# Optimization experiments

Measured on AMD Instinct MI355X. Metric: run time of the kernel, lower is better.

## Reference

```python
import jax, jax.numpy as jnp
import numpy as np

B, T, O, N, M, H = 64, 128, 256, 65536, 64, 512
EPS = 1e-8


def setup_inputs() -> dict:
    key = jax.random.key(0)
    ks = jax.random.split(key, 8)
    x = jax.random.normal(ks[0], (B, T, O, 1), dtype=jnp.float32)
    # original: memory.uniform_(1e-05, 0.0001)
    memory0 = jax.random.uniform(ks[1], (N, M), dtype=jnp.float32, minval=1e-5, maxval=1e-4)
    eye = jnp.eye(B, N, dtype=jnp.float32)  # torch.eye(batch_size, N)
    h0 = jnp.zeros((B, H), dtype=jnp.float32)
    Wxh = jax.random.normal(ks[2], (O, H), dtype=jnp.float32) * 0.05
    Wrh = jax.random.normal(ks[3], (M, H), dtype=jnp.float32) * 0.1
    bh = jnp.zeros((H,), dtype=jnp.float32)
    Wo = jax.random.normal(ks[4], (H, O), dtype=jnp.float32) * 0.05
    bo = jnp.zeros((O,), dtype=jnp.float32)
    rW = jax.random.normal(ks[5], (H, M + 6), dtype=jnp.float32) * 0.05
    rb = jnp.zeros((M + 6,), dtype=jnp.float32)
    wW = jax.random.normal(ks[6], (H, 3 * M + 6), dtype=jnp.float32) * 0.05
    wb = jnp.zeros((3 * M + 6,), dtype=jnp.float32)
    return dict(x=x, memory0=memory0, wr=eye, ww=eye, h0=h0, Wxh=Wxh, Wrh=Wrh,
                bh=bh, Wo=Wo, bo=bo, rW=rW, rb=rb, wW=wW, wb=wb)


def _address(head_out, w_prev, mem):
    """Graves-2014 NTM addressing. head_out: (B, M+6) raw head projection."""
    k = jnp.tanh(head_out[:, :M])                          # key       (B, M)
    beta = jax.nn.softplus(head_out[:, M:M + 1])           # strength  (B, 1)
    g = jax.nn.sigmoid(head_out[:, M + 1:M + 2])           # gate      (B, 1)
    s = jax.nn.softmax(head_out[:, M + 2:M + 5], axis=-1)  # shift     (B, 3)
    gamma = 1.0 + jax.nn.softplus(head_out[:, M + 5:M + 6])  # sharpen (B, 1)
    kn = k / (jnp.linalg.norm(k, axis=-1, keepdims=True) + EPS)
    mn = mem / (jnp.linalg.norm(mem, axis=-1, keepdims=True) + EPS)
    wc = jax.nn.softmax(beta * (kn @ mn.T), axis=-1)       # content   (B, N)
    wg = g * wc + (1.0 - g) * w_prev                       # interpolate
    # circular shift conv over N with taps {-1, 0, +1}
    wt = (s[:, 0:1] * jnp.roll(wg, 1, axis=1)
          + s[:, 1:2] * wg
          + s[:, 2:3] * jnp.roll(wg, -1, axis=1))
    wp = (wt + EPS) ** gamma                               # sharpen
    return wp / jnp.sum(wp, axis=1, keepdims=True)


def reference(x, memory0, wr, ww, h0, Wxh, Wrh, bh, Wo, bo, rW, rb, wW, wb):
    xt = jnp.transpose(x, (1, 0, 2, 3)).reshape(T, B, O)  # time-major, flattened
    inv_b = 1.0 / B

    def step(carry, x_t):
        mem, h = carry
        # write head: address, then erase/add (memory shared across batch -> mean)
        wh = h @ wW + wb                                   # (B, 3M+6)
        w_w = _address(wh[:, :M + 6], ww, mem)             # (B, N)
        e = jax.nn.sigmoid(wh[:, M + 6:2 * M + 6])         # (B, M)
        a = jnp.tanh(wh[:, 2 * M + 6:3 * M + 6])           # (B, M)
        erase = jnp.einsum('bn,bm->nm', w_w, e) * inv_b    # (N, M)
        add = jnp.einsum('bn,bm->nm', w_w, a) * inv_b
        m_t = mem * (1.0 - erase) + add
        # read head
        rh = h @ rW + rb                                   # (B, M+6)
        w_r = _address(rh, wr, m_t)                        # (B, N)
        r_t = w_r @ m_t                                    # (B, M)
        # feedforward controller step + output
        h_new = jax.nn.relu(x_t @ Wxh + r_t @ Wrh + bh)    # (B, H)
        out = jax.nn.sigmoid(h_new @ Wo + bo)              # (B, O)
        return (m_t, h_new), out

    (_, _), outs = jax.lax.scan(step, (memory0, h0), xt)   # outs: (T, B, O)
    return jnp.transpose(outs, (1, 0, 2))                  # (B, T, O)
```

## Files before the change

kernel.cpp:

```cpp
#include <hip/hip_runtime.h>

#define NROWS 65536
#define BB 64
#define TT 128
#define OO 256
#define MM 64
#define HH 512
#define EPSF 1e-8f

__device__ __forceinline__ float wredsum(float v) {
#pragma unroll
  for (int o = 1; o < 64; o <<= 1) v += __shfl_xor(v, o, 64);
  return v;
}
__device__ __forceinline__ float sigm(float x) { return 1.f / (1.f + __expf(-x)); }
__device__ __forceinline__ float softplus_(float x) { return x > 20.f ? x : log1pf(__expf(x)); }

__global__ void __launch_bounds__(256) k_xpre(const float* __restrict__ x, const float* __restrict__ Wxh,
                                              const float* __restrict__ bh, float* __restrict__ Xpre) {
  __shared__ float xl[4][256];
  int tid = threadIdx.x;
#pragma unroll
  for (int i = 0; i < 4; ++i) {
    int pair = blockIdx.x * 4 + i;
    int t = pair >> 6, b = pair & 63;
    xl[i][tid] = x[((size_t)b * TT + t) * OO + tid];
  }
  __syncthreads();
  for (int u = 0; u < 2; ++u) {
    int hh = tid + u * 256;
    float a[4];
    float bv = bh[hh];
#pragma unroll
    for (int i = 0; i < 4; ++i) a[i] = bv;
    for (int o = 0; o < 256; ++o) {
      float wv = Wxh[(size_t)o * HH + hh];
#pragma unroll
      for (int i = 0; i < 4; ++i) a[i] += xl[i][o] * wv;
    }
#pragma unroll
    for (int i = 0; i < 4; ++i) {
      int pair = blockIdx.x * 4 + i;
      Xpre[(size_t)pair * HH + hh] = a[i];
    }
  }
}

__global__ void __launch_bounds__(256) k_w1(const float* __restrict__ msrc, const float* __restrict__ knwT,
                                            const float* __restrict__ prmw, float* __restrict__ E,
                                            float* __restrict__ Swst, float* __restrict__ S2rst) {
  int tid = threadIdx.x, blk = blockIdx.x;
  int base = blk * 64;
  __shared__ float rows[4096];
  __shared__ float sred[256];
  if (blk == 0) {
    for (int i = tid; i < 32 * 64; i += 256) S2rst[i] = 0.f;
  }
  {
    const float4* s4 = (const float4*)(msrc + (size_t)base * 64);
    float4* d4 = (float4*)rows;
#pragma unroll
    for (int i = 0; i < 4; ++i) d4[tid + i * 256] = s4[tid + i * 256];
  }
  int l = tid & 63, w = tid >> 6;
  float kr[64];
#pragma unroll
  for (int j = 0; j < 64; ++j) kr[j] = knwT[j * 64 + l];
  float beta = prmw[l * 8 + 0];
  __syncthreads();
  float sacc = 0.f;
  for (int r = w * 16; r < w * 16 + 16; ++r) {
    const float4* row4 = (const float4*)(rows + r * 64);
    float dot = 0.f, nsq = 0.f;
#pragma unroll
    for (int j = 0; j < 16; ++j) {
      float4 rv = row4[j];
      dot += kr[j * 4] * rv.x + kr[j * 4 + 1] * rv.y + kr[j * 4 + 2] * rv.z + kr[j * 4 + 3] * rv.w;
      nsq += rv.x * rv.x + rv.y * rv.y + rv.z * rv.z + rv.w * rv.w;
    }
    float ev = __expf(beta * dot / (sqrtf(nsq) + EPSF) - beta);
    E[(size_t)(base + r) * 64 + l] = ev;
    sacc += ev;
  }
  sred[tid] = sacc;
  __syncthreads();
  if (tid < 64)
    atomicAdd(&Swst[(blk & 31) * 64 + tid], sred[tid] + sred[tid + 64] + sred[tid + 128] + sred[tid + 192]);
}

__global__ void __launch_bounds__(256) k_w2(const float* __restrict__ E, const float* __restrict__ prmw,
                                            const float* __restrict__ Swst, float* __restrict__ wpg,
                                            float* __restrict__ S2wst) {
  int tid = threadIdx.x, blk = blockIdx.x, base = blk * 64;
  __shared__ float EL[66 * 64];
  __shared__ float Sw[64];
  __shared__ float sred[256];
  if (tid < 64) {
    float s = 0.f;
    for (int st = 0; st < 32; ++st) s += Swst[st * 64 + tid];
    Sw[tid] = s;
  }
  for (int i = tid; i < 66 * 64; i += 256) {
    int rr = i >> 6, b2 = i & 63;
    EL[i] = E[(size_t)((base - 1 + rr) & (NROWS - 1)) * 64 + b2];
  }
  __syncthreads();
  int b = tid & 63, w = tid >> 6;
  float g = prmw[b * 8 + 1], gam = prmw[b * 8 + 2];
  float s0 = prmw[b * 8 + 3], s1 = prmw[b * 8 + 4], s2 = prmw[b * 8 + 5];
  float gi = g / Sw[b], gm1 = 1.f - g;
  float s2acc = 0.f;
  for (int i = 0; i < 16; ++i) {
    int ln = w + i * 4;
    int n = base + ln;
    int nm = (n - 1) & (NROWS - 1), np = (n + 1) & (NROWS - 1);
    float wgm = gi * EL[ln * 64 + b] + (nm == b ? gm1 : 0.f);
    float wgc = gi * EL[(ln + 1) * 64 + b] + (n == b ? gm1 : 0.f);
    float wgp = gi * EL[(ln + 2) * 64 + b] + (np == b ? gm1 : 0.f);
    float wt = s0 * wgm + s1 * wgc + s2 * wgp;
    float wp = __powf(wt + EPSF, gam);
    wpg[(size_t)n * 64 + b] = wp;
    s2acc += wp;
  }
  sred[tid] = s2acc;
  __syncthreads();
  if (tid < 64)
    atomicAdd(&S2wst[(blk & 31) * 64 + tid], sred[tid] + sred[tid + 64] + sred[tid + 128] + sred[tid + 192]);
}

__global__ void __launch_bounds__(256) k_w3(const float* __restrict__ msrc, float* __restrict__ mdst,
                                            const float* __restrict__ wpg, const float* __restrict__ ea2,
                                            const float* __restrict__ knrT, const float* __restrict__ prmr,
                                            const float* __restrict__ S2wst, float* __restrict__ E,
                                            float* __restrict__ Srst) {
  int tid = threadIdx.x, blk = blockIdx.x, base = blk * 64;
  __shared__ float2 ealds[4096];
  __shared__ float wlT[4 * 64 * 20];
  __shared__ float rowsN[4096];
  __shared__ float fb[64];
  __shared__ float sred[256];
  {
    const float4* s4 = (const float4*)ea2;
    float4* d4 = (float4*)ealds;
#pragma unroll
    for (int i = 0; i < 8; ++i) d4[tid + i * 256] = s4[tid + i * 256];
  }
  if (tid < 64) {
    float s = 0.f;
    for (int st = 0; st < 32; ++st) s += S2wst[st * 64 + tid];
    fb[tid] = 1.f / (64.f * s);
  }
  __syncthreads();
  int l = tid & 63, w = tid >> 6;
#pragma unroll
  for (int k = 0; k < 16; ++k) {
    float wv = wpg[(size_t)(base + w * 16 + k) * 64 + l] * fb[l];
    wlT[(w * 64 + l) * 20 + k] = wv;
  }
  __syncthreads();
  float er[16], ad[16];
#pragma unroll
  for (int k = 0; k < 16; ++k) { er[k] = 0.f; ad[k] = 0.f; }
  for (int b2 = 0; b2 < 64; ++b2) {
    float2 eav = ealds[b2 * 64 + l];
    const float4* wrow = (const float4*)(wlT + (w * 64 + b2) * 20);
    float4 q0 = wrow[0], q1 = wrow[1], q2 = wrow[2], q3 = wrow[3];
    float qa[16];
    qa[0] = q0.x; qa[1] = q0.y; qa[2] = q0.z; qa[3] = q0.w;
    qa[4] = q1.x; qa[5] = q1.y; qa[6] = q1.z; qa[7] = q1.w;
    qa[8] = q2.x; qa[9] = q2.y; qa[10] = q2.z; qa[11] = q2.w;
    qa[12] = q3.x; qa[13] = q3.y; qa[14] = q3.z; qa[15] = q3.w;
#pragma unroll
    for (int k = 0; k < 16; ++k) { er[k] += qa[k] * eav.x; ad[k] += qa[k] * eav.y; }
  }
#pragma unroll
  for (int k = 0; k < 16; ++k) {
    int r = w * 16 + k;
    size_t n = (size_t)(base + r);
    float mv = msrc[n * 64 + l];
    float nv = mv * (1.f - er[k]) + ad[k];
    mdst[n * 64 + l] = nv;
    rowsN[r * 64 + l] = nv;
  }
  __syncthreads();
  float kr[64];
#pragma unroll
  for (int j = 0; j < 64; ++j) kr[j] = knrT[j * 64 + l];
  float beta_r = prmr[l * 8 + 0];
  float sacc = 0.f;
  for (int r = w * 16; r < w * 16 + 16; ++r) {
    const float4* row4 = (const float4*)(rowsN + r * 64);
    float dot = 0.f, nsq = 0.f;
#pragma unroll
    for (int j = 0; j < 16; ++j) {
      float4 rv = row4[j];
      dot += kr[j * 4] * rv.x + kr[j * 4 + 1] * rv.y + kr[j * 4 + 2] * rv.z + kr[j * 4 + 3] * rv.w;
      nsq += rv.x * rv.x + rv.y * rv.y + rv.z * rv.z + rv.w * rv.w;
    }
    float ev = __expf(beta_r * dot / (sqrtf(nsq) + EPSF) - beta_r);
    E[(size_t)(base + r) * 64 + l] = ev;
    sacc += ev;
  }
  sred[tid] = sacc;
  __syncthreads();
  if (tid < 64)
    atomicAdd(&Srst[(blk & 31) * 64 + tid], sred[tid] + sred[tid + 64] + sred[tid + 128] + sred[tid + 192]);
}

__global__ void __launch_bounds__(256) k_r2(const float* __restrict__ E, const float* __restrict__ mdst,
                                            const float* __restrict__ prmr, const float* __restrict__ Srst,
                                            float* __restrict__ part, float* __restrict__ S2rst) {
  int tid = threadIdx.x, blk = blockIdx.x, base = blk * 64;
  __shared__ float mt[4096];
  __shared__ float EL[66 * 64];
  __shared__ float Sr[64];
  __shared__ float sred[256];
  __shared__ float racc[64 * 65];
  if (tid < 64) {
    float s = 0.f;
    for (int st = 0; st < 32; ++st) s += Srst[st * 64 + tid];
    Sr[tid] = s;
  }
  {
    const float4* s4 = (const float4*)(mdst + (size_t)base * 64);
    float4* d4 = (float4*)mt;
#pragma unroll
    for (int i = 0; i < 4; ++i) d4[tid + i * 256] = s4[tid + i * 256];
  }
  for (int i = tid; i < 66 * 64; i += 256) {
    int rr = i >> 6, b2 = i & 63;
    EL[i] = E[(size_t)((base - 1 + rr) & (NROWS - 1)) * 64 + b2];
  }
  __syncthreads();
  int b = tid & 63, w = tid >> 6;
  float g = prmr[b * 8 + 1], gam = prmr[b * 8 + 2];
  float s0 = prmr[b * 8 + 3], s1 = prmr[b * 8 + 4], s2 = prmr[b * 8 + 5];
  float gi = g / Sr[b], gm1 = 1.f - g;
  float acc[64];
#pragma unroll
  for (int m = 0; m < 64; ++m) acc[m] = 0.f;
  float s2acc = 0.f;
  for (int i = 0; i < 16; ++i) {
    int r = w * 16 + i;
    int n = base + r;
    int nm = (n - 1) & (NROWS - 1), np = (n + 1) & (NROWS - 1);
    float wgm = gi * EL[r * 64 + b] + (nm == b ? gm1 : 0.f);
    float wgc = gi * EL[(r + 1) * 64 + b] + (n == b ? gm1 : 0.f);
    float wgp = gi * EL[(r + 2) * 64 + b] + (np == b ? gm1 : 0.f);
    float wt = s0 * wgm + s1 * wgc + s2 * wgp;
    float wp = __powf(wt + EPSF, gam);
    s2acc += wp;
    const float4* row4 = (const float4*)(mt + r * 64);
#pragma unroll
    for (int m4 = 0; m4 < 16; ++m4) {
      float4 mv = row4[m4];
      acc[m4 * 4 + 0] += wp * mv.x;
      acc[m4 * 4 + 1] += wp * mv.y;
      acc[m4 * 4 + 2] += wp * mv.z;
      acc[m4 * 4 + 3] += wp * mv.w;
    }
  }
  sred[tid] = s2acc;
  __syncthreads();
  if (tid < 64)
    atomicAdd(&S2rst[(blk & 31) * 64 + tid], sred[tid] + sred[tid + 64] + sred[tid + 128] + sred[tid + 192]);
  if (w == 0) {
#pragma unroll
    for (int m = 0; m < 64; ++m) racc[b * 65 + m] = acc[m];
  }
  __syncthreads();
  for (int ww2 = 1; ww2 < 4; ++ww2) {
    if (w == ww2) {
#pragma unroll
      for (int m = 0; m < 64; ++m) racc[b * 65 + m] += acc[m];
    }
    __syncthreads();
  }
  for (int i = tid; i < 4096; i += 256) part[(size_t)blk * 4096 + i] = racc[(i >> 6) * 65 + (i & 63)];
}

__global__ void __launch_bounds__(512) k_cp(int t, const float* __restrict__ h0,
                                            const float* __restrict__ Xpre, float* __restrict__ Hbuf,
                                            const float* __restrict__ part, const float* __restrict__ S2rst,
                                            const float* __restrict__ Wrh, const float* __restrict__ wW,
                                            const float* __restrict__ wb, const float* __restrict__ rW,
                                            const float* __restrict__ rb, float* __restrict__ knwT,
                                            float* __restrict__ knrT, float* __restrict__ ea2,
                                            float* __restrict__ prmw, float* __restrict__ prmr,
                                            float* __restrict__ zst) {
  int b = blockIdx.x, tid = threadIdx.x;
  __shared__ float hl[512];
  __shared__ float proj[268];
  __shared__ float red[512];
  __shared__ float rt[64];
  __shared__ float s2r_sh;
  if (t >= 0) {
    float v = 0.f;
    if (tid < 32) v = S2rst[tid * 64 + b];
    if (tid < 64) red[tid] = v;
    __syncthreads();
    if (tid == 0) {
      float s = 0.f;
      for (int i = 0; i < 32; ++i) s += red[i];
      s2r_sh = s;
    }
    __syncthreads();
    {
      int m = tid & 63, q = tid >> 6;
      float acc = 0.f;
      for (int p = q; p < 1024; p += 8) acc += part[((size_t)p * 64 + b) * 64 + m];
      red[tid] = acc;
    }
    __syncthreads();
    if (tid < 64) {
      float r = 0.f;
#pragma unroll
      for (int q8 = 0; q8 < 8; ++q8) r += red[tid + q8 * 64];
      rt[tid] = r / s2r_sh;
    }
    __syncthreads();
    {
      int hh = tid;
      float a = Xpre[((size_t)t * 64 + b) * HH + hh];
      for (int m2 = 0; m2 < 64; ++m2) a += rt[m2] * Wrh[(size_t)m2 * HH + hh];
      a = fmaxf(a, 0.f);
      Hbuf[((size_t)t * 64 + b) * HH + hh] = a;
      hl[hh] = a;
    }
  } else {
    hl[tid] = h0[(size_t)b * HH + tid];
  }
  __syncthreads();
  if (b == 0) {
    for (int i = tid; i < 3 * 2048; i += 512) zst[i] = 0.f;
  }
  if (tid < 268) {
    int idx = tid;
    float a;
    if (idx < 198) {
      a = wb[idx];
      for (int hh = 0; hh < 512; ++hh) a += hl[hh] * wW[(size_t)hh * 198 + idx];
    } else {
      int jj = idx - 198;
      a = rb[jj];
      for (int hh = 0; hh < 512; ++hh) a += hl[hh] * rW[(size_t)hh * 70 + jj];
    }
    proj[idx] = a;
  }
  __syncthreads();
  int l = tid & 63, wv = tid >> 6;
  if (wv == 0) {
    float kv = tanhf(proj[l]);
    float s = wredsum(kv * kv);
    knwT[l * 64 + b] = kv / (sqrtf(s) + EPSF);
  } else if (wv == 1) {
    float kv = tanhf(proj[198 + l]);
    float s = wredsum(kv * kv);
    knrT[l * 64 + b] = kv / (sqrtf(s) + EPSF);
  } else if (wv == 2) {
    float ev = sigm(proj[70 + l]);
    float av = tanhf(proj[134 + l]);
    ((float2*)ea2)[b * 64 + l] = make_float2(ev, av);
  } else if (wv == 3) {
    if (l == 0) {
      float beta = softplus_(proj[64]);
      float g = sigm(proj[65]);
      float v0 = proj[66], v1 = proj[67], v2 = proj[68];
      float mx = fmaxf(v0, fmaxf(v1, v2));
      float e0 = __expf(v0 - mx), e1 = __expf(v1 - mx), e2 = __expf(v2 - mx);
      float is = 1.f / (e0 + e1 + e2);
      float gam = 1.f + softplus_(proj[69]);
      prmw[b * 8 + 0] = beta; prmw[b * 8 + 1] = g; prmw[b * 8 + 2] = gam;
      prmw[b * 8 + 3] = e0 * is; prmw[b * 8 + 4] = e1 * is; prmw[b * 8 + 5] = e2 * is;
    } else if (l == 1) {
      const int of = 198;
      float beta = softplus_(proj[of + 64]);
      float g = sigm(proj[of + 65]);
      float v0 = proj[of + 66], v1 = proj[of + 67], v2 = proj[of + 68];
      float mx = fmaxf(v0, fmaxf(v1, v2));
      float e0 = __expf(v0 - mx), e1 = __expf(v1 - mx), e2 = __expf(v2 - mx);
      float is = 1.f / (e0 + e1 + e2);
      float gam = 1.f + softplus_(proj[of + 69]);
      prmr[b * 8 + 0] = beta; prmr[b * 8 + 1] = g; prmr[b * 8 + 2] = gam;
      prmr[b * 8 + 3] = e0 * is; prmr[b * 8 + 4] = e1 * is; prmr[b * 8 + 5] = e2 * is;
    }
  }
}

__global__ void __launch_bounds__(256) k_out(const float* __restrict__ Hbuf, const float* __restrict__ Wo,
                                             const float* __restrict__ bo, float* __restrict__ out) {
  __shared__ float hl[4][512];
  int tid = threadIdx.x;
#pragma unroll
  for (int i = 0; i < 8; ++i) {
    int idx = tid + i * 256;
    hl[idx >> 9][idx & 511] = Hbuf[(size_t)blockIdx.x * 2048 + idx];
  }
  __syncthreads();
  float a[4];
  float bv = bo[tid];
#pragma unroll
  for (int i = 0; i < 4; ++i) a[i] = bv;
  for (int hh = 0; hh < 512; ++hh) {
    float wv = Wo[(size_t)hh * OO + tid];
#pragma unroll
    for (int i = 0; i < 4; ++i) a[i] += hl[i][hh] * wv;
  }
#pragma unroll
  for (int i = 0; i < 4; ++i) {
    int pair = blockIdx.x * 4 + i;
    int t = pair >> 6, b = pair & 63;
    out[((size_t)b * TT + t) * OO + tid] = 1.f / (1.f + __expf(-a[i]));
  }
}

extern "C" void kernel_launch(void* const* d_in, const int* in_sizes, int n_in,
                              void* d_out, int out_size, void* d_ws, size_t ws_size,
                              hipStream_t stream) {
  (void)in_sizes; (void)n_in; (void)out_size; (void)ws_size;
  const float* x    = (const float*)d_in[0];
  const float* mem0 = (const float*)d_in[1];
  const float* h0   = (const float*)d_in[4];
  const float* Wxh  = (const float*)d_in[5];
  const float* Wrh  = (const float*)d_in[6];
  const float* bh   = (const float*)d_in[7];
  const float* Wo   = (const float*)d_in[8];
  const float* bo   = (const float*)d_in[9];
  const float* rW   = (const float*)d_in[10];
  const float* rb   = (const float*)d_in[11];
  const float* wW   = (const float*)d_in[12];
  const float* wb   = (const float*)d_in[13];
  float* ws = (float*)d_ws;
  const size_t NM = (size_t)NROWS * MM;
  float* memA = ws;
  float* memB = memA + NM;
  float* E    = memB + NM;
  float* wpg  = E + NM;
  float* Xpre = wpg + NM;
  float* Hbuf = Xpre + NM;
  float* part = Hbuf + NM;
  float* small = part + NM;
  float* knwT = small;
  float* knrT = knwT + 4096;
  float* ea2  = knrT + 4096;
  float* prmw = ea2 + 8192;
  float* prmr = prmw + 512;
  float* Swst  = prmr + 512;
  float* S2wst = Swst + 2048;
  float* Srst  = S2wst + 2048;
  float* S2rst = Srst + 2048;

  hipMemcpyAsync(memA, mem0, NM * sizeof(float), hipMemcpyDeviceToDevice, stream);
  k_xpre<<<2048, 256, 0, stream>>>(x, Wxh, bh, Xpre);
  k_cp<<<64, 512, 0, stream>>>(-1, h0, Xpre, Hbuf, part, S2rst, Wrh, wW, wb, rW, rb,
                               knwT, knrT, ea2, prmw, prmr, Swst);
  for (int t = 0; t < TT; ++t) {
    float* msrc = (t & 1) ? memB : memA;
    float* mdst = (t & 1) ? memA : memB;
    k_w1<<<1024, 256, 0, stream>>>(msrc, knwT, prmw, E, Swst, S2rst);
    k_w2<<<1024, 256, 0, stream>>>(E, prmw, Swst, wpg, S2wst);
    k_w3<<<1024, 256, 0, stream>>>(msrc, mdst, wpg, ea2, knrT, prmr, S2wst, E, Srst);
    k_r2<<<1024, 256, 0, stream>>>(E, mdst, prmr, Srst, part, S2rst);
    k_cp<<<64, 512, 0, stream>>>(t, h0, Xpre, Hbuf, part, S2rst, Wrh, wW, wb, rW, rb,
                                 knwT, knrT, ea2, prmw, prmr, Swst);
  }
  k_out<<<2048, 256, 0, stream>>>(Hbuf, Wo, bo, (float*)d_out);
}
```

Measured before the change: 25.10 ms.

## Recompute content weights in-block instead of storing E and wpg buffers

Drops the global wpg buffer and the E write in k_w3. k_w3 now recomputes the write-head content exponentials (with a one-row halo) and the sharpened weights from memory rows in shared memory. k_r2 likewise recomputes the read content exponentials from mdst rather than reading E. This trades extra dot-product and exp work, plus halo rows, for fewer full N×B global reads and writes per timestep, and reads ea2 straight from global memory instead of staging it in LDS.

```diff
diff --git a/kernel.cpp b/kernel.cpp
--- a/kernel.cpp
+++ b/kernel.cpp
@@ -89,8 +89,7 @@
 }
 
 __global__ void __launch_bounds__(256) k_w2(const float* __restrict__ E, const float* __restrict__ prmw,
-                                            const float* __restrict__ Swst, float* __restrict__ wpg,
-                                            float* __restrict__ S2wst) {
+                                            const float* __restrict__ Swst, float* __restrict__ S2wst) {
   int tid = threadIdx.x, blk = blockIdx.x, base = blk * 64;
   __shared__ float EL[66 * 64];
   __shared__ float Sw[64];
@@ -118,9 +117,7 @@
     float wgc = gi * EL[(ln + 1) * 64 + b] + (n == b ? gm1 : 0.f);
     float wgp = gi * EL[(ln + 2) * 64 + b] + (np == b ? gm1 : 0.f);
     float wt = s0 * wgm + s1 * wgc + s2 * wgp;
-    float wp = __powf(wt + EPSF, gam);
-    wpg[(size_t)n * 64 + b] = wp;
-    s2acc += wp;
+    s2acc += __powf(wt + EPSF, gam);
   }
   sred[tid] = s2acc;
   __syncthreads();
@@ -129,67 +126,31 @@
 }
 
 __global__ void __launch_bounds__(256) k_w3(const float* __restrict__ msrc, float* __restrict__ mdst,
-                                            const float* __restrict__ wpg, const float* __restrict__ ea2,
-                                            const float* __restrict__ knrT, const float* __restrict__ prmr,
-                                            const float* __restrict__ S2wst, float* __restrict__ E,
-                                            float* __restrict__ Srst) {
+                                            const float* __restrict__ ea2, const float* __restrict__ knwT,
+                                            const float* __restrict__ knrT, const float* __restrict__ prmw,
+                                            const float* __restrict__ prmr, const float* __restrict__ Swst,
+                                            const float* __restrict__ S2wst, float* __restrict__ Srst) {
   int tid = threadIdx.x, blk = blockIdx.x, base = blk * 64;
-  __shared__ float2 ealds[4096];
-  __shared__ float wlT[4 * 64 * 20];
-  __shared__ float rowsN[4096];
-  __shared__ float fb[64];
+  __shared__ float rows[66 * 64];
+  __shared__ float EL[66 * 64];
   __shared__ float sred[256];
-  {
-    const float4* s4 = (const float4*)ea2;
-    float4* d4 = (float4*)ealds;
-#pragma unroll
-    for (int i = 0; i < 8; ++i) d4[tid + i * 256] = s4[tid + i * 256];
-  }
-  if (tid < 64) {
-    float s = 0.f;
-    for (int st = 0; st < 32; ++st) s += S2wst[st * 64 + tid];
-    fb[tid] = 1.f / (64.f * s);
-  }
-  __syncthreads();
   int l = tid & 63, w = tid >> 6;
-#pragma unroll
-  for (int k = 0; k < 16; ++k) {
-    float wv = wpg[(size_t)(base + w * 16 + k) * 64 + l] * fb[l];
-    wlT[(w * 64 + l) * 20 + k] = wv;
-  }
-  __syncthreads();
-  float er[16], ad[16];
-#pragma unroll
-  for (int k = 0; k < 16; ++k) { er[k] = 0.f; ad[k] = 0.f; }
-  for (int b2 = 0; b2 < 64; ++b2) {
-    float2 eav = ealds[b2 * 64 + l];
-    const float4* wrow = (const float4*)(wlT + (w * 64 + b2) * 20);
-    float4 q0 = wrow[0], q1 = wrow[1], q2 = wrow[2], q3 = wrow[3];
-    float qa[16];
-    qa[0] = q0.x; qa[1] = q0.y; qa[2] = q0.z; qa[3] = q0.w;
-    qa[4] = q1.x; qa[5] = q1.y; qa[6] = q1.z; qa[7] = q1.w;
-    qa[8] = q2.x; qa[9] = q2.y; qa[10] = q2.z; qa[11] = q2.w;
-    qa[12] = q3.x; qa[13] = q3.y; qa[14] = q3.z; qa[15] = q3.w;
-#pragma unroll
-    for (int k = 0; k < 16; ++k) { er[k] += qa[k] * eav.x; ad[k] += qa[k] * eav.y; }
-  }
-#pragma unroll
-  for (int k = 0; k < 16; ++k) {
-    int r = w * 16 + k;
-    size_t n = (size_t)(base + r);
-    float mv = msrc[n * 64 + l];
-    float nv = mv * (1.f - er[k]) + ad[k];
-    mdst[n * 64 + l] = nv;
-    rowsN[r * 64 + l] = nv;
-  }
-  __syncthreads();
+  for (int i = tid; i < 66 * 64; i += 256) {
+    int rr = i >> 6, b2 = i & 63;
+    rows[i] = msrc[(size_t)((base - 1 + rr) & (NROWS - 1)) * 64 + b2];
+  }
   float kr[64];
 #pragma unroll
-  for (int j = 0; j < 64; ++j) kr[j] = knrT[j * 64 + l];
-  float beta_r = prmr[l * 8 + 0];
-  float sacc = 0.f;
-  for (int r = w * 16; r < w * 16 + 16; ++r) {
-    const float4* row4 = (const float4*)(rowsN + r * 64);
+  for (int j = 0; j < 64; ++j) kr[j] = knwT[j * 64 + l];
+  float beta = prmw[l * 8 + 0];
+  float Swl = 0.f, S2wl = 0.f;
+  for (int st = 0; st < 32; ++st) { Swl += Swst[st * 64 + l]; S2wl += S2wst[st * 64 + l]; }
+  __syncthreads();
+  for (int k = 0; k < 17; ++k) {
+    int r;
+    if (k < 16) r = w * 16 + k;
+    else { if (w >= 2) break; r = 64 + w; }
+    const float4* row4 = (const float4*)(rows + r * 64);
     float dot = 0.f, nsq = 0.f;
 #pragma unroll
     for (int j = 0; j < 16; ++j) {
@@ -197,9 +158,65 @@
       dot += kr[j * 4] * rv.x + kr[j * 4 + 1] * rv.y + kr[j * 4 + 2] * rv.z + kr[j * 4 + 3] * rv.w;
       nsq += rv.x * rv.x + rv.y * rv.y + rv.z * rv.z + rv.w * rv.w;
     }
-    float ev = __expf(beta_r * dot / (sqrtf(nsq) + EPSF) - beta_r);
-    E[(size_t)(base + r) * 64 + l] = ev;
-    sacc += ev;
+    EL[r * 64 + l] = __expf(beta * dot / (sqrtf(nsq) + EPSF) - beta);
+  }
+  __syncthreads();
+  float g = prmw[l * 8 + 1], gam = prmw[l * 8 + 2];
+  float s0 = prmw[l * 8 + 3], s1 = prmw[l * 8 + 4], s2 = prmw[l * 8 + 5];
+  float gi = g / Swl, gm1 = 1.f - g;
+  float fbl = 1.f / (64.f * S2wl);
+  float wpreg[16];
+#pragma unroll
+  for (int k = 0; k < 16; ++k) {
+    int r = w * 16 + k;
+    int n = base + r;
+    int nm = (n - 1) & (NROWS - 1), np = (n + 1) & (NROWS - 1);
+    float wgm = gi * EL[r * 64 + l] + (nm == l ? gm1 : 0.f);
+    float wgc = gi * EL[(r + 1) * 64 + l] + (n == l ? gm1 : 0.f);
+    float wgp = gi * EL[(r + 2) * 64 + l] + (np == l ? gm1 : 0.f);
+    float wt = s0 * wgm + s1 * wgc + s2 * wgp;
+    wpreg[k] = __powf(wt + EPSF, gam) * fbl;
+  }
+  __syncthreads();
+  float* wpn = EL;
+#pragma unroll
+  for (int k = 0; k < 16; ++k) wpn[(w * 16 + k) * 64 + l] = wpreg[k];
+  __syncthreads();
+  float er[16], ad[16];
+#pragma unroll
+  for (int k = 0; k < 16; ++k) { er[k] = 0.f; ad[k] = 0.f; }
+  for (int b2 = 0; b2 < 64; ++b2) {
+    float2 eav = ((const float2*)ea2)[b2 * 64 + l];
+#pragma unroll
+    for (int k = 0; k < 16; ++k) {
+      float wpb = wpn[(w * 16 + k) * 64 + b2];
+      er[k] += wpb * eav.x;
+      ad[k] += wpb * eav.y;
+    }
+  }
+#pragma unroll
+  for (int k = 0; k < 16; ++k) {
+    int r = w * 16 + k;
+    float mv = rows[(r + 1) * 64 + l];
+    float nv = mv * (1.f - er[k]) + ad[k];
+    mdst[(size_t)(base + r) * 64 + l] = nv;
+    rows[(r + 1) * 64 + l] = nv;
+  }
+  __syncthreads();
+#pragma unroll
+  for (int j = 0; j < 64; ++j) kr[j] = knrT[j * 64 + l];
+  float beta_r = prmr[l * 8 + 0];
+  float sacc = 0.f;
+  for (int k = 0; k < 16; ++k) {
+    const float4* row4 = (const float4*)(rows + (w * 16 + k + 1) * 64);
+    float dot = 0.f, nsq = 0.f;
+#pragma unroll
+    for (int j = 0; j < 16; ++j) {
+      float4 rv = row4[j];
+      dot += kr[j * 4] * rv.x + kr[j * 4 + 1] * rv.y + kr[j * 4 + 2] * rv.z + kr[j * 4 + 3] * rv.w;
+      nsq += rv.x * rv.x + rv.y * rv.y + rv.z * rv.z + rv.w * rv.w;
+    }
+    sacc += __expf(beta_r * dot / (sqrtf(nsq) + EPSF) - beta_r);
   }
   sred[tid] = sacc;
   __syncthreads();
@@ -207,35 +224,47 @@
     atomicAdd(&Srst[(blk & 31) * 64 + tid], sred[tid] + sred[tid + 64] + sred[tid + 128] + sred[tid + 192]);
 }
 
-__global__ void __launch_bounds__(256) k_r2(const float* __restrict__ E, const float* __restrict__ mdst,
+__global__ void __launch_bounds__(256) k_r2(const float* __restrict__ mdst, const float* __restrict__ knrT,
                                             const float* __restrict__ prmr, const float* __restrict__ Srst,
                                             float* __restrict__ part, float* __restrict__ S2rst) {
   int tid = threadIdx.x, blk = blockIdx.x, base = blk * 64;
-  __shared__ float mt[4096];
+  __shared__ float mt[66 * 64];
   __shared__ float EL[66 * 64];
   __shared__ float Sr[64];
   __shared__ float sred[256];
-  __shared__ float racc[64 * 65];
+  int l = tid & 63, w = tid >> 6;
+  for (int i = tid; i < 66 * 64; i += 256) {
+    int rr = i >> 6, b2 = i & 63;
+    mt[i] = mdst[(size_t)((base - 1 + rr) & (NROWS - 1)) * 64 + b2];
+  }
   if (tid < 64) {
     float s = 0.f;
     for (int st = 0; st < 32; ++st) s += Srst[st * 64 + tid];
     Sr[tid] = s;
   }
-  {
-    const float4* s4 = (const float4*)(mdst + (size_t)base * 64);
-    float4* d4 = (float4*)mt;
-#pragma unroll
-    for (int i = 0; i < 4; ++i) d4[tid + i * 256] = s4[tid + i * 256];
-  }
-  for (int i = tid; i < 66 * 64; i += 256) {
-    int rr = i >> 6, b2 = i & 63;
-    EL[i] = E[(size_t)((base - 1 + rr) & (NROWS - 1)) * 64 + b2];
-  }
-  __syncthreads();
-  int b = tid & 63, w = tid >> 6;
-  float g = prmr[b * 8 + 1], gam = prmr[b * 8 + 2];
-  float s0 = prmr[b * 8 + 3], s1 = prmr[b * 8 + 4], s2 = prmr[b * 8 + 5];
-  float gi = g / Sr[b], gm1 = 1.f - g;
+  float kr[64];
+#pragma unroll
+  for (int j = 0; j < 64; ++j) kr[j] = knrT[j * 64 + l];
+  float beta_r = prmr[l * 8 + 0];
+  __syncthreads();
+  for (int k = 0; k < 17; ++k) {
+    int r;
+    if (k < 16) r = w * 16 + k;
+    else { if (w >= 2) break; r = 64 + w; }
+    const float4* row4 = (const float4*)(mt + r * 64);
+    float dot = 0.f, nsq = 0.f;
+#pragma unroll
+    for (int j = 0; j < 16; ++j) {
+      float4 rv = row4[j];
+      dot += kr[j * 4] * rv.x + kr[j * 4 + 1] * rv.y + kr[j * 4 + 2] * rv.z + kr[j * 4 + 3] * rv.w;
+      nsq += rv.x * rv.x + rv.y * rv.y + rv.z * rv.z + rv.w * rv.w;
+    }
+    EL[r * 64 + l] = __expf(beta_r * dot / (sqrtf(nsq) + EPSF) - beta_r);
+  }
+  __syncthreads();
+  float g = prmr[l * 8 + 1], gam = prmr[l * 8 + 2];
+  float s0 = prmr[l * 8 + 3], s1 = prmr[l * 8 + 4], s2 = prmr[l * 8 + 5];
+  float gi = g / Sr[l], gm1 = 1.f - g;
   float acc[64];
 #pragma unroll
   for (int m = 0; m < 64; ++m) acc[m] = 0.f;
@@ -244,13 +273,13 @@
     int r = w * 16 + i;
     int n = base + r;
     int nm = (n - 1) & (NROWS - 1), np = (n + 1) & (NROWS - 1);
-    float wgm = gi * EL[r * 64 + b] + (nm == b ? gm1 : 0.f);
-    float wgc = gi * EL[(r + 1) * 64 + b] + (n == b ? gm1 : 0.f);
-    float wgp = gi * EL[(r + 2) * 64 + b] + (np == b ? gm1 : 0.f);
+    float wgm = gi * EL[r * 64 + l] + (nm == l ? gm1 : 0.f);
+    float wgc = gi * EL[(r + 1) * 64 + l] + (n == l ? gm1 : 0.f);
+    float wgp = gi * EL[(r + 2) * 64 + l] + (np == l ? gm1 : 0.f);
     float wt = s0 * wgm + s1 * wgc + s2 * wgp;
     float wp = __powf(wt + EPSF, gam);
     s2acc += wp;
-    const float4* row4 = (const float4*)(mt + r * 64);
+    const float4* row4 = (const float4*)(mt + (r + 1) * 64);
 #pragma unroll
     for (int m4 = 0; m4 < 16; ++m4) {
       float4 mv = row4[m4];
@@ -264,15 +293,16 @@
   __syncthreads();
   if (tid < 64)
     atomicAdd(&S2rst[(blk & 31) * 64 + tid], sred[tid] + sred[tid + 64] + sred[tid + 128] + sred[tid + 192]);
+  float* racc = EL;
   if (w == 0) {
 #pragma unroll
-    for (int m = 0; m < 64; ++m) racc[b * 65 + m] = acc[m];
+    for (int m = 0; m < 64; ++m) racc[l * 65 + m] = acc[m];
   }
   __syncthreads();
   for (int ww2 = 1; ww2 < 4; ++ww2) {
     if (w == ww2) {
 #pragma unroll
-      for (int m = 0; m < 64; ++m) racc[b * 65 + m] += acc[m];
+      for (int m = 0; m < 64; ++m) racc[l * 65 + m] += acc[m];
     }
     __syncthreads();
   }
@@ -435,8 +465,7 @@
   float* memA = ws;
   float* memB = memA + NM;
   float* E    = memB + NM;
-  float* wpg  = E + NM;
-  float* Xpre = wpg + NM;
+  float* Xpre = E + NM;
   float* Hbuf = Xpre + NM;
   float* part = Hbuf + NM;
   float* small = part + NM;
@@ -458,9 +487,9 @@
     float* msrc = (t & 1) ? memB : memA;
     float* mdst = (t & 1) ? memA : memB;
     k_w1<<<1024, 256, 0, stream>>>(msrc, knwT, prmw, E, Swst, S2rst);
-    k_w2<<<1024, 256, 0, stream>>>(E, prmw, Swst, wpg, S2wst);
-    k_w3<<<1024, 256, 0, stream>>>(msrc, mdst, wpg, ea2, knrT, prmr, S2wst, E, Srst);
-    k_r2<<<1024, 256, 0, stream>>>(E, mdst, prmr, Srst, part, S2rst);
+    k_w2<<<1024, 256, 0, stream>>>(E, prmw, Swst, S2wst);
+    k_w3<<<1024, 256, 0, stream>>>(msrc, mdst, ea2, knwT, knrT, prmw, prmr, Swst, S2wst, Srst);
+    k_r2<<<1024, 256, 0, stream>>>(mdst, knrT, prmr, Srst, part, S2rst);
     k_cp<<<64, 512, 0, stream>>>(t, h0, Xpre, Hbuf, part, S2rst, Wrh, wW, wb, rW, rb,
                                  knwT, knrT, ea2, prmw, prmr, Swst);
   }
```

New measurement: 34.89 ms. +39.0%, slower.
